# Optimization experiments

Hardware: AMD Instinct MI355X
Metric: run time of the kernel (lower is better)

Reference implementation:

```python
import jax, jax.numpy as jnp
import numpy as np


def _grid_edges(hh, ww):
    """Directed 4-neighbor grid edges over an hh x ww patch grid, plus self-loops
    (PyG gcn_norm adds self-loops with weight 1)."""
    idx = np.arange(hh * ww).reshape(hh, ww)
    src = np.concatenate([idx[1:].ravel(), idx[:-1].ravel(), idx[:, 1:].ravel(), idx[:, :-1].ravel()])
    dst = np.concatenate([idx[:-1].ravel(), idx[1:].ravel(), idx[:, :-1].ravel(), idx[:, 1:].ravel()])
    loops = np.arange(hh * ww)
    return np.concatenate([src, loops]), np.concatenate([dst, loops])


def setup_inputs() -> dict:
    key = jax.random.key(0)
    k1, k2, k3, k4 = jax.random.split(key, 4)
    B, C, H, W = 4, 3, 512, 512
    E = 192
    p = 2
    x = jax.random.normal(k1, (B, C, H, W), dtype=jnp.float32)
    conv_w = jax.random.normal(k2, (E, C, p, p), dtype=jnp.float32) * (1.0 / np.sqrt(C * p * p))
    gcn_w = jax.random.normal(k3, (E, E), dtype=jnp.float32) * (1.0 / np.sqrt(E))
    gcn_b = jax.random.normal(k4, (E,), dtype=jnp.float32) * 0.02
    return {"x": x, "conv_w": conv_w, "gcn_w": gcn_w, "gcn_b": gcn_b}


def reference(x, conv_w, gcn_w, gcn_b):
    B, C, H, W = x.shape
    E, _, p, _ = conv_w.shape
    hh, ww = H // p, W // p
    N = hh * ww

    # Conv2d(kernel=stride=p, bias=False) == patchify + linear projection.
    xr = x.reshape(B, C, hh, p, ww, p)
    feats = jnp.einsum('bciujv,ecuv->bije', xr, conv_w).reshape(B, N, E)  # [B, N, E]

    # Grid graph (shared across batch), with self-loops.
    src_np, dst_np = _grid_edges(hh, ww)
    src = jnp.asarray(src_np, dtype=jnp.int32)
    dst = jnp.asarray(dst_np, dtype=jnp.int32)

    # GCNConv: out = D^{-1/2} (A + I) D^{-1/2} (X W^T) + b
    deg = jax.ops.segment_sum(jnp.ones(src.shape[0], feats.dtype), dst, num_segments=N)
    dinv = jax.lax.rsqrt(deg)  # deg >= 1 due to self-loops
    norm = dinv[src] * dinv[dst]  # [Etot]

    xw = jnp.einsum('bnc,oc->bno', feats, gcn_w)  # linear (PyG stores W as [out, in])
    msgs = xw[:, src, :] * norm[None, :, None]  # gather + scale: [B, Etot, E]
    agg = jax.vmap(lambda m: jax.ops.segment_sum(m, dst, num_segments=N))(msgs)  # scatter-sum
    return agg + gcn_b  # [B, N, E]
```

## Files before the change

kernel.cpp:

```cpp
#include <hip/hip_runtime.h>
#include <cstddef>

constexpr int kH  = 512, kW = 512, kC = 3;
constexpr int kHH = 256, kWW = 256;
constexpr int kN  = kHH * kWW;
constexpr int kE  = 192, kK = 12, kB = 4;

__device__ __forceinline__ float dinvf(int i, int j) {
    int deg = 1 + (i > 0) + (i < kHH - 1) + (j > 0) + (j < kWW - 1);
    return rsqrtf((float)deg);
}

__global__ __launch_bounds__(64) void build_M(const float* __restrict__ gcn_w,
                                              const float* __restrict__ conv_w,
                                              float* __restrict__ M) {
    const int e = blockIdx.x;
    const int lane = threadIdx.x;
    float acc[kK];
#pragma unroll
    for (int k = 0; k < kK; ++k) acc[k] = 0.f;
    for (int j = lane; j < kE; j += 64) {
        const float g = gcn_w[e * kE + j];
        const float4 c0 = *(const float4*)(conv_w + j * kK + 0);
        const float4 c1 = *(const float4*)(conv_w + j * kK + 4);
        const float4 c2 = *(const float4*)(conv_w + j * kK + 8);
        acc[0] += g * c0.x; acc[1] += g * c0.y; acc[2]  += g * c0.z; acc[3]  += g * c0.w;
        acc[4] += g * c1.x; acc[5] += g * c1.y; acc[6]  += g * c1.z; acc[7]  += g * c1.w;
        acc[8] += g * c2.x; acc[9] += g * c2.y; acc[10] += g * c2.z; acc[11] += g * c2.w;
    }
#pragma unroll
    for (int k = 0; k < kK; ++k) {
        float v = acc[k];
#pragma unroll
        for (int off = 32; off > 0; off >>= 1) v += __shfl_down(v, off);
        if (lane == 0) M[e * kK + k] = v;
    }
}

constexpr int TI = 8, TJ = 8, TNODES = TI * TJ;
constexpr int THREADS = 192;

__global__ __launch_bounds__(THREADS) void fused_gcn(
        const float* __restrict__ x, const float* __restrict__ M,
        const float* __restrict__ bias, float* __restrict__ out) {
    __shared__ float s_aggp[TNODES][kK];

    const int t = threadIdx.x;
    const int nbj = kWW / TJ;
    const int nbi = kHH / TI;
    const int blk = blockIdx.x;
    const int bj = blk % nbj;
    const int bi = (blk / nbj) % nbi;
    const int b  = blk / (nbj * nbi);
    const int i0 = bi * TI, j0 = bj * TJ;

    const int e4  = t % 48;
    const int sub = t / 48;
    const int e   = e4 * 4;
    float4 mrow[12];
#pragma unroll
    for (int r = 0; r < 12; ++r) mrow[r] = ((const float4*)(M + (size_t)e * kK))[r];
    const float4 bv = *(const float4*)(bias + e);

#pragma unroll
    for (int q = 0; q < (TNODES * kK) / THREADS; ++q) {
        const int entry = t + q * THREADS;
        const int nl = entry / kK;
        const int k  = entry % kK;
        const int i = i0 + nl / TJ;
        const int j = j0 + nl % TJ;
        const int c = k >> 2, u = (k >> 1) & 1, v = k & 1;
        const float* xb = x + ((size_t)(b * kC + c) * kH + u) * kW + v;
        const float dc = dinvf(i, j);
        float sum = dc * xb[(2 * i) * kW + 2 * j];
        if (i > 0)       sum += dinvf(i - 1, j) * xb[(2 * i - 2) * kW + 2 * j];
        if (i < kHH - 1) sum += dinvf(i + 1, j) * xb[(2 * i + 2) * kW + 2 * j];
        if (j > 0)       sum += dinvf(i, j - 1) * xb[(2 * i) * kW + 2 * j - 2];
        if (j < kWW - 1) sum += dinvf(i, j + 1) * xb[(2 * i) * kW + 2 * j + 2];
        s_aggp[nl][k] = dc * sum;
    }
    __syncthreads();

#pragma unroll 4
    for (int it = 0; it < TNODES / 4; ++it) {
        const int nl = it * 4 + sub;
        const float4 a0 = *((const float4*)&s_aggp[nl][0]);
        const float4 a1 = *((const float4*)&s_aggp[nl][4]);
        const float4 a2 = *((const float4*)&s_aggp[nl][8]);
        float4 acc;
        float* accp = (float*)&acc;
#pragma unroll
        for (int r = 0; r < 4; ++r) {
            const float4 m0 = mrow[r * 3 + 0];
            const float4 m1 = mrow[r * 3 + 1];
            const float4 m2 = mrow[r * 3 + 2];
            float s = ((const float*)&bv)[r];
            s += m0.x * a0.x + m0.y * a0.y + m0.z * a0.z + m0.w * a0.w;
            s += m1.x * a1.x + m1.y * a1.y + m1.z * a1.z + m1.w * a1.w;
            s += m2.x * a2.x + m2.y * a2.y + m2.z * a2.z + m2.w * a2.w;
            accp[r] = s;
        }
        const int i = i0 + nl / TJ;
        const int j = j0 + nl % TJ;
        const size_t n = (size_t)i * kWW + j;
        float4* op = (float4*)(out + ((size_t)b * kN + n) * kE + e);
        *op = acc;
    }
}

extern "C" void kernel_launch(void* const* d_in, const int* in_sizes, int n_in,
                              void* d_out, int out_size, void* d_ws, size_t ws_size,
                              hipStream_t stream) {
    const float* x      = (const float*)d_in[0];
    const float* conv_w = (const float*)d_in[1];
    const float* gcn_w  = (const float*)d_in[2];
    const float* gcn_b  = (const float*)d_in[3];
    float* out = (float*)d_out;
    float* M   = (float*)d_ws;

    build_M<<<kE, 64, 0, stream>>>(gcn_w, conv_w, M);
    fused_gcn<<<kB * (kHH / TI) * (kWW / TJ), THREADS, 0, stream>>>(x, M, gcn_b, out);
}
```

Baseline: 242.2 us.

## Process one patch row per block with shared-memory staged input and nontemporal stores

Each block now handles a full row of 256 patch nodes instead of an 8x8 tile. The six input rows per channel it needs are staged into shared memory with coalesced float4 loads, and the stencil aggregation reads from LDS instead of making scattered global loads. Output writes use nontemporal stores so the large output stream bypasses cache retention. The trade-offs are more LDS per block, fewer blocks (1024) and a longer serial output loop per block.

```diff
diff --git a/kernel.cpp b/kernel.cpp
--- a/kernel.cpp
+++ b/kernel.cpp
@@ -5,6 +5,8 @@
 constexpr int kHH = 256, kWW = 256;
 constexpr int kN  = kHH * kWW;
 constexpr int kE  = 192, kK = 12, kB = 4;
+
+typedef float nt_f4 __attribute__((ext_vector_type(4)));
 
 __device__ __forceinline__ float dinvf(int i, int j) {
     int deg = 1 + (i > 0) + (i < kHH - 1) + (j > 0) + (j < kWW - 1);
@@ -37,22 +39,18 @@
     }
 }
 
-constexpr int TI = 8, TJ = 8, TNODES = TI * TJ;
 constexpr int THREADS = 192;
+constexpr int ROWPAD  = 516;
 
 __global__ __launch_bounds__(THREADS) void fused_gcn(
         const float* __restrict__ x, const float* __restrict__ M,
         const float* __restrict__ bias, float* __restrict__ out) {
-    __shared__ float s_aggp[TNODES][kK];
+    __shared__ float s_x[kC][6][ROWPAD];
+    __shared__ float s_aggp[kWW][kK];
 
     const int t = threadIdx.x;
-    const int nbj = kWW / TJ;
-    const int nbi = kHH / TI;
-    const int blk = blockIdx.x;
-    const int bj = blk % nbj;
-    const int bi = (blk / nbj) % nbi;
-    const int b  = blk / (nbj * nbi);
-    const int i0 = bi * TI, j0 = bj * TJ;
+    const int i = blockIdx.x % kHH;
+    const int b = blockIdx.x / kHH;
 
     const int e4  = t % 48;
     const int sub = t / 48;
@@ -62,33 +60,48 @@
     for (int r = 0; r < 12; ++r) mrow[r] = ((const float4*)(M + (size_t)e * kK))[r];
     const float4 bv = *(const float4*)(bias + e);
 
+    const int r0 = 2 * i - 2;
 #pragma unroll
-    for (int q = 0; q < (TNODES * kK) / THREADS; ++q) {
-        const int entry = t + q * THREADS;
-        const int nl = entry / kK;
-        const int k  = entry % kK;
-        const int i = i0 + nl / TJ;
-        const int j = j0 + nl % TJ;
-        const int c = k >> 2, u = (k >> 1) & 1, v = k & 1;
-        const float* xb = x + ((size_t)(b * kC + c) * kH + u) * kW + v;
-        const float dc = dinvf(i, j);
-        float sum = dc * xb[(2 * i) * kW + 2 * j];
-        if (i > 0)       sum += dinvf(i - 1, j) * xb[(2 * i - 2) * kW + 2 * j];
-        if (i < kHH - 1) sum += dinvf(i + 1, j) * xb[(2 * i + 2) * kW + 2 * j];
-        if (j > 0)       sum += dinvf(i, j - 1) * xb[(2 * i) * kW + 2 * j - 2];
-        if (j < kWW - 1) sum += dinvf(i, j + 1) * xb[(2 * i) * kW + 2 * j + 2];
-        s_aggp[nl][k] = dc * sum;
+    for (int q = 0; q < 12; ++q) {
+        const int idx  = t + q * THREADS;
+        const int cr   = idx >> 7;
+        const int col4 = idx & 127;
+        const int c = cr / 6, row = cr % 6;
+        const int rg = r0 + row;
+        float4 val = make_float4(0.f, 0.f, 0.f, 0.f);
+        if (rg >= 0 && rg < kH)
+            val = *(const float4*)(x + (((size_t)(b * kC + c) * kH + rg) * kW) + col4 * 4);
+        *(float4*)&s_x[c][row][col4 * 4] = val;
     }
     __syncthreads();
 
+#pragma unroll
+    for (int q = 0; q < 16; ++q) {
+        const int idx = t + q * THREADS;
+        const int j   = idx / kK;
+        const int k   = idx % kK;
+        const int c = k >> 2, u = (k >> 1) & 1, v = k & 1;
+        const int col = 2 * j + v;
+        const float dc = dinvf(i, j);
+        const float du = dinvf(i - 1, j);
+        const float dd = dinvf(i + 1, j);
+        float sum = dc * s_x[c][u + 2][col]
+                  + du * s_x[c][u][col]
+                  + dd * s_x[c][u + 4][col];
+        if (j > 0)       sum += dinvf(i, j - 1) * s_x[c][u + 2][col - 2];
+        if (j < kWW - 1) sum += dinvf(i, j + 1) * s_x[c][u + 2][col + 2];
+        s_aggp[j][k] = dc * sum;
+    }
+    __syncthreads();
+
+    float* outb = out + ((size_t)b * kN + (size_t)i * kWW) * kE + e;
 #pragma unroll 4
-    for (int it = 0; it < TNODES / 4; ++it) {
+    for (int it = 0; it < kWW / 4; ++it) {
         const int nl = it * 4 + sub;
         const float4 a0 = *((const float4*)&s_aggp[nl][0]);
         const float4 a1 = *((const float4*)&s_aggp[nl][4]);
         const float4 a2 = *((const float4*)&s_aggp[nl][8]);
-        float4 acc;
-        float* accp = (float*)&acc;
+        nt_f4 acc;
 #pragma unroll
         for (int r = 0; r < 4; ++r) {
             const float4 m0 = mrow[r * 3 + 0];
@@ -98,13 +111,9 @@
             s += m0.x * a0.x + m0.y * a0.y + m0.z * a0.z + m0.w * a0.w;
             s += m1.x * a1.x + m1.y * a1.y + m1.z * a1.z + m1.w * a1.w;
             s += m2.x * a2.x + m2.y * a2.y + m2.z * a2.z + m2.w * a2.w;
-            accp[r] = s;
+            acc[r] = s;
         }
-        const int i = i0 + nl / TJ;
-        const int j = j0 + nl % TJ;
-        const size_t n = (size_t)i * kWW + j;
-        float4* op = (float4*)(out + ((size_t)b * kN + n) * kE + e);
-        *op = acc;
+        __builtin_nontemporal_store(acc, (nt_f4*)(outb + (size_t)nl * kE));
     }
 }
 
@@ -119,5 +128,5 @@
     float* M   = (float*)d_ws;
 
     build_M<<<kE, 64, 0, stream>>>(gcn_w, conv_w, M);
-    fused_gcn<<<kB * (kHH / TI) * (kWW / TJ), THREADS, 0, stream>>>(x, M, gcn_b, out);
+    fused_gcn<<<kB * kHH, THREADS, 0, stream>>>(x, M, gcn_b, out);
 }
```

New measurement: 230.8 us. -4.7%, faster.
